# Kernel optimization log

Measured on AMD Instinct MI355X. Metric: run time of the kernel, lower is better.

## Reference

```python
import jax, jax.numpy as jnp
import numpy as np

POOLSCALE = 4  # HSA: avg-pool kernel/stride = (scale, scale*4)

def _avg_pool(x, kh, kw):
    # kernel == stride and dims divisible -> exact reshape-mean pooling
    B, C, H, W = x.shape
    return x.reshape(B, C, H // kh, kh, W // kw, kw).mean(axis=(3, 5))

def setup_inputs() -> dict:
    key = jax.random.key(0)
    k1, k2, k3 = jax.random.split(key, 3)
    shape = (4, 64, 192, 192)
    return {
        "K": jax.random.normal(k1, shape, dtype=jnp.float32),
        "Q": jax.random.normal(k2, shape, dtype=jnp.float32),
        "V": jax.random.normal(k3, shape, dtype=jnp.float32),
    }

def reference(K, Q, V):
    B, C, H, W = Q.shape
    kh, kw = POOLSCALE, POOLSCALE * 4
    Qp = Q.reshape(B, C, H * W).transpose(0, 2, 1)          # [B, HW, C]
    Kp = _avg_pool(K, kh, kw)                               # [B, C, h, w]
    Kp = Kp.reshape(B, C, -1)                               # [B, C, hw_p]
    Vp = _avg_pool(V, kh, kw).reshape(B, C, -1)             # [B, C, hw_p]
    scores = jnp.einsum('bnc,bcm->bnm', Qp, Kp)             # [B, HW, hw_p]
    attn = jax.nn.softmax(scores, axis=1)                   # softmax over query dim (dim=1), as in torch code
    out = jnp.einsum('bcm,bnm->bcn', Vp, attn)              # V_pie @ attn^T -> [B, C, HW]
    return out.reshape(B, C, H, W)
```

## Files before the change

### kernel.cpp

```cpp
#include <hip/hip_runtime.h>

#define BB 4
#define CC 64
#define HH 192
#define WW 192
#define HWN (HH*WW)
#define KH 4
#define KW 16
#define PW (WW/KW)
#define MP ((HH/KH)*(WW/KW))
#define NT 128
#define MT 64
#define MITER (MP/MT)
#define SCALE_W 65536.0f
#define INV_SCALE (1.0f/65536.0f)

typedef _Float16 half8 __attribute__((ext_vector_type(8)));
typedef _Float16 half4 __attribute__((ext_vector_type(4)));
typedef float floatx4 __attribute__((ext_vector_type(4)));


__global__ __launch_bounds__(256) void pool_kernel(
    const float* __restrict__ Kin, const float* __restrict__ Vin,
    _Float16* __restrict__ kptF, float* __restrict__ vp) {
  int t = blockIdx.x * 256 + threadIdx.x;
  const int total = BB * CC * MP;
  bool isV = t >= total;
  int idx = isV ? t - total : t;
  int m = idx % MP;
  int c = (idx / MP) % CC;
  int b = idx / (MP * CC);
  int mh = m / PW, mw = m % PW;
  const float* src = (isV ? Vin : Kin) + (((b * CC + c) * HH + mh * KH) * WW + mw * KW);
  float s = 0.f;
#pragma unroll
  for (int r = 0; r < KH; ++r) {
    const float4* row = (const float4*)(src + r * WW);
#pragma unroll
    for (int j = 0; j < KW / 4; ++j) {
      float4 v = row[j];
      s += v.x + v.y + v.z + v.w;
    }
  }
  s *= (1.0f / (KH * KW));
  if (isV) {
    vp[(b * CC + c) * MP + m] = s;
  } else {
    int mi = m >> 6, mloc = m & 63, l15 = mloc >> 2, mf = mloc & 3;
    int ks = c >> 5, lhi = (c >> 3) & 3, e = c & 7;
    int lane = lhi * 16 + l15;
    kptF[(((((b * MITER + mi) * 4 + mf) * 2 + ks)) * 64 + lane) * 8 + e] = (_Float16)s;
  }
}

__global__ __launch_bounds__(256) void colsum_kernel(
    const float* __restrict__ Q, const _Float16* __restrict__ kptF,
    float* __restrict__ colsum) {
  __shared__ float cs[MP];
  int b = blockIdx.y;
  int n0 = blockIdx.x * NT;
  int tid = threadIdx.x;
  int wv = tid >> 6;
  int lane = tid & 63;
  int l15 = lane & 15, lhi = lane >> 4;

  for (int i = tid; i < MP; i += 256) cs[i] = 0.f;
  __syncthreads();

  const float* Qb = Q + b * CC * HWN;
  int nrow = n0 + wv * 32 + l15;
  half8 afrag[2][2];
#pragma unroll
  for (int nf = 0; nf < 2; ++nf)
#pragma unroll
    for (int ks = 0; ks < 2; ++ks) {
      int cbase = ks * 32 + lhi * 8;
      int n = nrow + nf * 16;
#pragma unroll
      for (int e = 0; e < 8; ++e)
        afrag[nf][ks][e] = (_Float16)Qb[(cbase + e) * HWN + n];
    }

  const _Float16* kb = kptF + b * MITER * 8 * 512;
  floatx4 zero = {0.f, 0.f, 0.f, 0.f};

  half8 bb[2][4][2];
  floatx4 sacc[2][2][4];

#pragma unroll
  for (int mf = 0; mf < 4; ++mf)
#pragma unroll
    for (int ks = 0; ks < 2; ++ks)
      bb[0][mf][ks] = *(const half8*)(kb + ((0 * 4 + mf) * 2 + ks) * 512 + lane * 8);
#pragma unroll
  for (int mf = 0; mf < 4; ++mf)
#pragma unroll
    for (int ks = 0; ks < 2; ++ks)
      bb[1][mf][ks] = *(const half8*)(kb + ((1 * 4 + mf) * 2 + ks) * 512 + lane * 8);

#pragma unroll
  for (int nf = 0; nf < 2; ++nf)
#pragma unroll
    for (int mf = 0; mf < 4; ++mf) sacc[0][nf][mf] = zero;
  __builtin_amdgcn_s_setprio(1);
#pragma unroll
  for (int ks = 0; ks < 2; ++ks)
#pragma unroll
    for (int nf = 0; nf < 2; ++nf)
#pragma unroll
      for (int mf = 0; mf < 4; ++mf)
        sacc[0][nf][mf] = __builtin_amdgcn_mfma_f32_16x16x32_f16(
            afrag[nf][ks], bb[0][mf][ks], sacc[0][nf][mf], 0, 0, 0);
  __builtin_amdgcn_s_setprio(0);

#pragma unroll
  for (int mi = 1; mi <= 8; ++mi) {
    int cur = mi & 1, prv = (mi - 1) & 1;
    if (mi + 1 <= 8) {
#pragma unroll
      for (int mf = 0; mf < 4; ++mf)
#pragma unroll
        for (int ks = 0; ks < 2; ++ks)
          bb[(mi + 1) & 1][mf][ks] =
              *(const half8*)(kb + (((mi + 1) * 4 + mf) * 2 + ks) * 512 + lane * 8);
    }
#pragma unroll
    for (int nf = 0; nf < 2; ++nf)
#pragma unroll
      for (int mf = 0; mf < 4; ++mf) sacc[cur][nf][mf] = zero;
    __builtin_amdgcn_s_setprio(1);
#pragma unroll
    for (int ks = 0; ks < 2; ++ks)
#pragma unroll
      for (int nf = 0; nf < 2; ++nf)
#pragma unroll
        for (int mf = 0; mf < 4; ++mf)
          sacc[cur][nf][mf] = __builtin_amdgcn_mfma_f32_16x16x32_f16(
              afrag[nf][ks], bb[cur][mf][ks], sacc[cur][nf][mf], 0, 0, 0);
    __builtin_amdgcn_s_setprio(0);
#pragma unroll
    for (int mf = 0; mf < 4; ++mf) {
      float s = 0.f;
#pragma unroll
      for (int nf = 0; nf < 2; ++nf)
#pragma unroll
        for (int r = 0; r < 4; ++r)
          s += __expf(sacc[prv][nf][mf][r]);
      s += __shfl_xor(s, 16);
      s += __shfl_xor(s, 32);
      if (lane < 16) atomicAdd(&cs[(mi - 1) * MT + l15 * 4 + mf], s);
    }
  }
#pragma unroll
  for (int mf = 0; mf < 4; ++mf) {
    float s = 0.f;
#pragma unroll
    for (int nf = 0; nf < 2; ++nf)
#pragma unroll
      for (int r = 0; r < 4; ++r)
        s += __expf(sacc[0][nf][mf][r]);
    s += __shfl_xor(s, 16);
    s += __shfl_xor(s, 32);
    if (lane < 16) atomicAdd(&cs[8 * MT + l15 * 4 + mf], s);
  }
  __syncthreads();
  for (int i = tid; i < MP; i += 256) atomicAdd(&colsum[b * MP + i], cs[i]);
}

__global__ __launch_bounds__(256) void wprep_kernel(
    const float* __restrict__ vp, const float* __restrict__ colsum,
    _Float16* __restrict__ wqF) {
  int t = blockIdx.x * 256 + threadIdx.x;
  int m = t % MP;
  int c = (t / MP) % CC;
  int b = t / (CC * MP);
  float w = vp[t] / colsum[b * MP + m] * SCALE_W;
  int cf = c >> 4, l15 = c & 15;
  int mi = m >> 6, mloc = m & 63;
  int ks = mloc >> 5, lhi = (mloc >> 3) & 3, e = mloc & 7;
  int lane = lhi * 16 + l15;
  wqF[((((b * MITER + mi) * 4 + cf) * 2 + ks) * 64 + lane) * 8 + e] = (_Float16)w;
}

__global__ __launch_bounds__(256) void attn_main_kernel(
    const float* __restrict__ Q, const _Float16* __restrict__ kptF,
    const _Float16* __restrict__ wqF, float* __restrict__ out) {
  __shared__ char elds[4 * 8192];
  int b = blockIdx.y;
  int n0 = blockIdx.x * NT;
  int tid = threadIdx.x;
  int wv = tid >> 6;
  int lane = tid & 63;
  int l15 = lane & 15, lhi = lane >> 4;
  char* eb0 = elds + wv * 8192;
  char* eb1 = eb0 + 4096;

  const float* Qb = Q + b * CC * HWN;
  int nrow = n0 + wv * 32 + l15;
  half8 afrag[2][2];
#pragma unroll
  for (int nf = 0; nf < 2; ++nf)
#pragma unroll
    for (int ks = 0; ks < 2; ++ks) {
      int cbase = ks * 32 + lhi * 8;
      int n = nrow + nf * 16;
#pragma unroll
      for (int e = 0; e < 8; ++e)
        afrag[nf][ks][e] = (_Float16)Qb[(cbase + e) * HWN + n];
    }

  floatx4 zero = {0.f, 0.f, 0.f, 0.f};
  floatx4 oacc[4][2];
#pragma unroll
  for (int cf = 0; cf < 4; ++cf)
#pragma unroll
    for (int nf = 0; nf < 2; ++nf) oacc[cf][nf] = zero;

  const _Float16* kb = kptF + b * MITER * 8 * 512;
  const _Float16* wb = wqF + b * MITER * 8 * 512;

  half8 bb[2][4][2];
  half8 ww[2][4][2];
  floatx4 sacc[2][4];

#pragma unroll
  for (int mf = 0; mf < 4; ++mf)
#pragma unroll
    for (int ks = 0; ks < 2; ++ks)
      bb[0][mf][ks] = *(const half8*)(kb + ((0 * 4 + mf) * 2 + ks) * 512 + lane * 8);
#pragma unroll
  for (int cf = 0; cf < 4; ++cf)
#pragma unroll
    for (int ks = 0; ks < 2; ++ks)
      ww[0][cf][ks] = *(const half8*)(wb + ((0 * 4 + cf) * 2 + ks) * 512 + lane * 8);

#pragma unroll
  for (int mf = 0; mf < 4; ++mf)
#pragma unroll
    for (int ks = 0; ks < 2; ++ks)
      bb[1][mf][ks] = *(const half8*)(kb + ((1 * 4 + mf) * 2 + ks) * 512 + lane * 8);
#pragma unroll
  for (int nf = 0; nf < 2; ++nf)
#pragma unroll
    for (int mf = 0; mf < 4; ++mf) sacc[nf][mf] = zero;
  __builtin_amdgcn_s_setprio(1);
#pragma unroll
  for (int ks = 0; ks < 2; ++ks)
#pragma unroll
    for (int nf = 0; nf < 2; ++nf)
#pragma unroll
      for (int mf = 0; mf < 4; ++mf)
        sacc[nf][mf] = __builtin_amdgcn_mfma_f32_16x16x32_f16(
            afrag[nf][ks], bb[0][mf][ks], sacc[nf][mf], 0, 0, 0);
  __builtin_amdgcn_s_setprio(0);
#pragma unroll
  for (int nf = 0; nf < 2; ++nf)
#pragma unroll
    for (int r = 0; r < 4; ++r) {
      int nl = nf * 16 + lhi * 4 + r;
      half4 h;
#pragma unroll
      for (int mf = 0; mf < 4; ++mf) h[mf] = (_Float16)__expf(sacc[nf][mf][r]);
      int byte = nl * 128 + ((((l15 >> 1) ^ (nl & 7))) << 4) + ((l15 & 1) << 3);
      *(half4*)(eb0 + byte) = h;
    }

#pragma unroll
  for (int mi = 1; mi <= 8; ++mi) {
    int cur = mi & 1, prv = (mi - 1) & 1;
    char* ebR = prv ? eb1 : eb0;
    char* ebW = cur ? eb1 : eb0;

    half8 ef[2][2];
#pragma unroll
    for (int nf = 0; nf < 2; ++nf)
#pragma unroll
      for (int ks = 0; ks < 2; ++ks) {
        int nl = nf * 16 + l15;
        int slot = (ks * 4 + lhi) ^ (nl & 7);
        ef[nf][ks] = *(const half8*)(ebR + nl * 128 + (slot << 4));
      }

    if (mi + 1 <= 8) {
#pragma unroll
      for (int mf = 0; mf < 4; ++mf)
#pragma unroll
        for (int ks = 0; ks < 2; ++ks)
          bb[(mi + 1) & 1][mf][ks] =
              *(const half8*)(kb + (((mi + 1) * 4 + mf) * 2 + ks) * 512 + lane * 8);
    }

#pragma unroll
    for (int nf = 0; nf < 2; ++nf)
#pragma unroll
      for (int mf = 0; mf < 4; ++mf) sacc[nf][mf] = zero;
    __builtin_amdgcn_s_setprio(1);
#pragma unroll
    for (int ks = 0; ks < 2; ++ks)
#pragma unroll
      for (int nf = 0; nf < 2; ++nf)
#pragma unroll
        for (int mf = 0; mf < 4; ++mf)
          sacc[nf][mf] = __builtin_amdgcn_mfma_f32_16x16x32_f16(
              afrag[nf][ks], bb[cur][mf][ks], sacc[nf][mf], 0, 0, 0);

#pragma unroll
    for (int ks = 0; ks < 2; ++ks)
#pragma unroll
      for (int cf = 0; cf < 4; ++cf)
#pragma unroll
        for (int nf = 0; nf < 2; ++nf)
          oacc[cf][nf] = __builtin_amdgcn_mfma_f32_16x16x32_f16(
              ww[prv][cf][ks], ef[nf][ks], oacc[cf][nf], 0, 0, 0);
    __builtin_amdgcn_s_setprio(0);

#pragma unroll
    for (int cf = 0; cf < 4; ++cf)
#pragma unroll
      for (int ks = 0; ks < 2; ++ks)
        ww[cur][cf][ks] = *(const half8*)(wb + ((mi * 4 + cf) * 2 + ks) * 512 + lane * 8);

#pragma unroll
    for (int nf = 0; nf < 2; ++nf)
#pragma unroll
      for (int r = 0; r < 4; ++r) {
        int nl = nf * 16 + lhi * 4 + r;
        half4 h;
#pragma unroll
        for (int mf = 0; mf < 4; ++mf) h[mf] = (_Float16)__expf(sacc[nf][mf][r]);
        int byte = nl * 128 + ((((l15 >> 1) ^ (nl & 7))) << 4) + ((l15 & 1) << 3);
        *(half4*)(ebW + byte) = h;
      }
  }

  {
    half8 ef[2][2];
#pragma unroll
    for (int nf = 0; nf < 2; ++nf)
#pragma unroll
      for (int ks = 0; ks < 2; ++ks) {
        int nl = nf * 16 + l15;
        int slot = (ks * 4 + lhi) ^ (nl & 7);
        ef[nf][ks] = *(const half8*)(eb0 + nl * 128 + (slot << 4));
      }
    __builtin_amdgcn_s_setprio(1);
#pragma unroll
    for (int ks = 0; ks < 2; ++ks)
#pragma unroll
      for (int cf = 0; cf < 4; ++cf)
#pragma unroll
        for (int nf = 0; nf < 2; ++nf)
          oacc[cf][nf] = __builtin_amdgcn_mfma_f32_16x16x32_f16(
              ww[0][cf][ks], ef[nf][ks], oacc[cf][nf], 0, 0, 0);
    __builtin_amdgcn_s_setprio(0);
  }

  float* ob = out + b * CC * HWN;
#pragma unroll
  for (int cf = 0; cf < 4; ++cf)
#pragma unroll
    for (int nf = 0; nf < 2; ++nf)
#pragma unroll
      for (int r = 0; r < 4; ++r) {
        int c = cf * 16 + lhi * 4 + r;
        int n = n0 + wv * 32 + nf * 16 + l15;
        ob[c * HWN + n] = oacc[cf][nf][r] * INV_SCALE;
      }
}

extern "C" void kernel_launch(void* const* d_in, const int* in_sizes, int n_in,
                              void* d_out, int out_size, void* d_ws, size_t ws_size,
                              hipStream_t stream) {
  const float* K = (const float*)d_in[0];
  const float* Q = (const float*)d_in[1];
  const float* V = (const float*)d_in[2];
  float* out = (float*)d_out;
  char* ws = (char*)d_ws;
  _Float16* kptF  = (_Float16*)(ws);
  float*    vp    = (float*)(ws + 294912);
  _Float16* wqF   = (_Float16*)(ws + 294912 + 589824);
  float*    colsum = (float*)(ws + 294912 + 589824 + 294912);

  hipMemsetAsync(colsum, 0, BB * MP * sizeof(float), stream);
  pool_kernel<<<(2 * BB * CC * MP) / 256, 256, 0, stream>>>(K, V, kptF, vp);
  colsum_kernel<<<dim3(HWN / NT, BB), 256, 0, stream>>>(Q, kptF, colsum);
  wprep_kernel<<<(BB * CC * MP) / 256, 256, 0, stream>>>(vp, colsum, wqF);
  attn_main_kernel<<<dim3(HWN / NT, BB), 256, 0, stream>>>(Q, kptF, wqF, out);
}
```

Measured before the change: 101.9 us.

## Stage K and W tiles into LDS with async global_load_lds triple buffering

In both the colsum and main attention kernels, every wave used to load the per-batch K (and W) fragments from global memory into its own registers. Now the block loads them cooperatively into a 3-stage LDS ring using direct global-to-LDS loads, with vmcnt waits and block barriers between stages, so each tile is fetched once per block instead of once per wave. The colsum kernel also drops the cross-lane shuffle reduction and lets every lane atomically add into the shared column sums. The cost is more LDS traffic and LDS atomics, an extra barrier per iteration, and a possible race: a wave can start overwriting a stage slot before other waves have finished reading it.

New measurement: 133.1 us. +30.5%, slower.

```diff
diff --git a/kernel.cpp b/kernel.cpp
--- a/kernel.cpp
+++ b/kernel.cpp
@@ -1,4 +1,5 @@
 #include <hip/hip_runtime.h>
+#include <stdint.h>
 
 #define BB 4
 #define CC 64
@@ -19,6 +20,13 @@
 typedef _Float16 half4 __attribute__((ext_vector_type(4)));
 typedef float floatx4 __attribute__((ext_vector_type(4)));
 
+static __device__ __forceinline__ void gload16(const void* g, void* l) {
+  __builtin_amdgcn_global_load_lds((const __attribute__((address_space(1))) void*)g,
+                                   (__attribute__((address_space(3))) void*)l, 16, 0, 0);
+}
+#define WAITCNT_VM(N) asm volatile("s_waitcnt vmcnt(" #N ")" ::: "memory")
+#define WAITCNT_LGKM0 asm volatile("s_waitcnt lgkmcnt(0)" ::: "memory")
+
 
 __global__ __launch_bounds__(256) void pool_kernel(
     const float* __restrict__ Kin, const float* __restrict__ Vin,
@@ -57,6 +65,7 @@
     const float* __restrict__ Q, const _Float16* __restrict__ kptF,
     float* __restrict__ colsum) {
   __shared__ float cs[MP];
+  __shared__ char stg[3 * 8192];
   int b = blockIdx.y;
   int n0 = blockIdx.x * NT;
   int tid = threadIdx.x;
@@ -65,7 +74,6 @@
   int l15 = lane & 15, lhi = lane >> 4;
 
   for (int i = tid; i < MP; i += 256) cs[i] = 0.f;
-  __syncthreads();
 
   const float* Qb = Q + b * CC * HWN;
   int nrow = n0 + wv * 32 + l15;
@@ -82,61 +90,50 @@
     }
 
   const _Float16* kb = kptF + b * MITER * 8 * 512;
+  {
+    int q0 = wv * 2;
+#pragma unroll
+    for (int j = 0; j < 2; ++j)
+      gload16(kb + 0 * 4096 + (q0 + j) * 512 + lane * 8, stg + 0 * 8192 + (q0 + j) * 1024);
+#pragma unroll
+    for (int j = 0; j < 2; ++j)
+      gload16(kb + 1 * 4096 + (q0 + j) * 512 + lane * 8, stg + 1 * 8192 + (q0 + j) * 1024);
+  }
+  WAITCNT_LGKM0;
+  WAITCNT_VM(2);
+  __builtin_amdgcn_sched_barrier(0);
+  __builtin_amdgcn_s_barrier();
+
   floatx4 zero = {0.f, 0.f, 0.f, 0.f};
-
-  half8 bb[2][4][2];
-  floatx4 sacc[2][2][4];
-
-#pragma unroll
-  for (int mf = 0; mf < 4; ++mf)
+#pragma unroll
+  for (int mi = 0; mi < MITER; ++mi) {
+    half8 bfr[4][2];
+#pragma unroll
+    for (int mf = 0; mf < 4; ++mf)
+#pragma unroll
+      for (int ks = 0; ks < 2; ++ks)
+        bfr[mf][ks] = *(const half8*)(stg + (mi % 3) * 8192 + (mf * 2 + ks) * 1024 + lane * 16);
+    if (mi + 2 < MITER) {
+      int q0 = wv * 2;
+#pragma unroll
+      for (int j = 0; j < 2; ++j)
+        gload16(kb + (mi + 2) * 4096 + (q0 + j) * 512 + lane * 8,
+                stg + ((mi + 2) % 3) * 8192 + (q0 + j) * 1024);
+    }
+    floatx4 sacc[2][4];
+#pragma unroll
+    for (int nf = 0; nf < 2; ++nf)
+#pragma unroll
+      for (int mf = 0; mf < 4; ++mf) sacc[nf][mf] = zero;
+    __builtin_amdgcn_s_setprio(1);
 #pragma unroll
     for (int ks = 0; ks < 2; ++ks)
-      bb[0][mf][ks] = *(const half8*)(kb + ((0 * 4 + mf) * 2 + ks) * 512 + lane * 8);
-#pragma unroll
-  for (int mf = 0; mf < 4; ++mf)
-#pragma unroll
-    for (int ks = 0; ks < 2; ++ks)
-      bb[1][mf][ks] = *(const half8*)(kb + ((1 * 4 + mf) * 2 + ks) * 512 + lane * 8);
-
-#pragma unroll
-  for (int nf = 0; nf < 2; ++nf)
-#pragma unroll
-    for (int mf = 0; mf < 4; ++mf) sacc[0][nf][mf] = zero;
-  __builtin_amdgcn_s_setprio(1);
-#pragma unroll
-  for (int ks = 0; ks < 2; ++ks)
-#pragma unroll
-    for (int nf = 0; nf < 2; ++nf)
-#pragma unroll
-      for (int mf = 0; mf < 4; ++mf)
-        sacc[0][nf][mf] = __builtin_amdgcn_mfma_f32_16x16x32_f16(
-            afrag[nf][ks], bb[0][mf][ks], sacc[0][nf][mf], 0, 0, 0);
-  __builtin_amdgcn_s_setprio(0);
-
-#pragma unroll
-  for (int mi = 1; mi <= 8; ++mi) {
-    int cur = mi & 1, prv = (mi - 1) & 1;
-    if (mi + 1 <= 8) {
-#pragma unroll
-      for (int mf = 0; mf < 4; ++mf)
-#pragma unroll
-        for (int ks = 0; ks < 2; ++ks)
-          bb[(mi + 1) & 1][mf][ks] =
-              *(const half8*)(kb + (((mi + 1) * 4 + mf) * 2 + ks) * 512 + lane * 8);
-    }
-#pragma unroll
-    for (int nf = 0; nf < 2; ++nf)
-#pragma unroll
-      for (int mf = 0; mf < 4; ++mf) sacc[cur][nf][mf] = zero;
-    __builtin_amdgcn_s_setprio(1);
-#pragma unroll
-    for (int ks = 0; ks < 2; ++ks)
 #pragma unroll
       for (int nf = 0; nf < 2; ++nf)
 #pragma unroll
         for (int mf = 0; mf < 4; ++mf)
-          sacc[cur][nf][mf] = __builtin_amdgcn_mfma_f32_16x16x32_f16(
-              afrag[nf][ks], bb[cur][mf][ks], sacc[cur][nf][mf], 0, 0, 0);
+          sacc[nf][mf] = __builtin_amdgcn_mfma_f32_16x16x32_f16(
+              afrag[nf][ks], bfr[mf][ks], sacc[nf][mf], 0, 0, 0);
     __builtin_amdgcn_s_setprio(0);
 #pragma unroll
     for (int mf = 0; mf < 4; ++mf) {
@@ -145,23 +142,14 @@
       for (int nf = 0; nf < 2; ++nf)
 #pragma unroll
         for (int r = 0; r < 4; ++r)
-          s += __expf(sacc[prv][nf][mf][r]);
-      s += __shfl_xor(s, 16);
-      s += __shfl_xor(s, 32);
-      if (lane < 16) atomicAdd(&cs[(mi - 1) * MT + l15 * 4 + mf], s);
-    }
-  }
-#pragma unroll
-  for (int mf = 0; mf < 4; ++mf) {
-    float s = 0.f;
-#pragma unroll
-    for (int nf = 0; nf < 2; ++nf)
-#pragma unroll
-      for (int r = 0; r < 4; ++r)
-        s += __expf(sacc[0][nf][mf][r]);
-    s += __shfl_xor(s, 16);
-    s += __shfl_xor(s, 32);
-    if (lane < 16) atomicAdd(&cs[8 * MT + l15 * 4 + mf], s);
+          s += __expf(sacc[nf][mf][r]);
+      atomicAdd(&cs[mi * MT + l15 * 4 + mf], s);
+    }
+    if (mi < MITER - 1) {
+      if (mi + 2 < MITER) { WAITCNT_VM(2); } else { WAITCNT_VM(0); }
+      __builtin_amdgcn_sched_barrier(0);
+      __builtin_amdgcn_s_barrier();
+    }
   }
   __syncthreads();
   for (int i = tid; i < MP; i += 256) atomicAdd(&colsum[b * MP + i], cs[i]);
@@ -185,14 +173,15 @@
 __global__ __launch_bounds__(256) void attn_main_kernel(
     const float* __restrict__ Q, const _Float16* __restrict__ kptF,
     const _Float16* __restrict__ wqF, float* __restrict__ out) {
-  __shared__ char elds[4 * 8192];
+  __shared__ char lds[3 * 16384 + 4 * 8192];
+  char* stg = lds;
   int b = blockIdx.y;
   int n0 = blockIdx.x * NT;
   int tid = threadIdx.x;
   int wv = tid >> 6;
   int lane = tid & 63;
   int l15 = lane & 15, lhi = lane >> 4;
-  char* eb0 = elds + wv * 8192;
+  char* eb0 = lds + 49152 + wv * 8192;
   char* eb1 = eb0 + 4096;
 
   const float* Qb = Q + b * CC * HWN;
@@ -219,77 +208,62 @@
   const _Float16* kb = kptF + b * MITER * 8 * 512;
   const _Float16* wb = wqF + b * MITER * 8 * 512;
 
-  half8 bb[2][4][2];
-  half8 ww[2][4][2];
-  floatx4 sacc[2][4];
-
-#pragma unroll
-  for (int mf = 0; mf < 4; ++mf)
-#pragma unroll
-    for (int ks = 0; ks < 2; ++ks)
-      bb[0][mf][ks] = *(const half8*)(kb + ((0 * 4 + mf) * 2 + ks) * 512 + lane * 8);
-#pragma unroll
-  for (int cf = 0; cf < 4; ++cf)
-#pragma unroll
-    for (int ks = 0; ks < 2; ++ks)
-      ww[0][cf][ks] = *(const half8*)(wb + ((0 * 4 + cf) * 2 + ks) * 512 + lane * 8);
-
-#pragma unroll
-  for (int mf = 0; mf < 4; ++mf)
-#pragma unroll
-    for (int ks = 0; ks < 2; ++ks)
-      bb[1][mf][ks] = *(const half8*)(kb + ((1 * 4 + mf) * 2 + ks) * 512 + lane * 8);
-#pragma unroll
-  for (int nf = 0; nf < 2; ++nf)
-#pragma unroll
-    for (int mf = 0; mf < 4; ++mf) sacc[nf][mf] = zero;
-  __builtin_amdgcn_s_setprio(1);
-#pragma unroll
-  for (int ks = 0; ks < 2; ++ks)
-#pragma unroll
-    for (int nf = 0; nf < 2; ++nf)
-#pragma unroll
-      for (int mf = 0; mf < 4; ++mf)
-        sacc[nf][mf] = __builtin_amdgcn_mfma_f32_16x16x32_f16(
-            afrag[nf][ks], bb[0][mf][ks], sacc[nf][mf], 0, 0, 0);
-  __builtin_amdgcn_s_setprio(0);
-#pragma unroll
-  for (int nf = 0; nf < 2; ++nf)
-#pragma unroll
-    for (int r = 0; r < 4; ++r) {
-      int nl = nf * 16 + lhi * 4 + r;
-      half4 h;
-#pragma unroll
-      for (int mf = 0; mf < 4; ++mf) h[mf] = (_Float16)__expf(sacc[nf][mf][r]);
-      int byte = nl * 128 + ((((l15 >> 1) ^ (nl & 7))) << 4) + ((l15 & 1) << 3);
-      *(half4*)(eb0 + byte) = h;
-    }
-
-#pragma unroll
-  for (int mi = 1; mi <= 8; ++mi) {
-    int cur = mi & 1, prv = (mi - 1) & 1;
-    char* ebR = prv ? eb1 : eb0;
-    char* ebW = cur ? eb1 : eb0;
-
+#define STAGE_T(t, s)                                                          \
+  {                                                                            \
+    int q0_ = wv * 4;                                                          \
+    _Pragma("unroll") for (int j_ = 0; j_ < 4; ++j_) {                         \
+      int q_ = q0_ + j_;                                                       \
+      const _Float16* srcp_ = (q_ < 8 ? kb + (t)*4096 + q_ * 512               \
+                                      : wb + (t)*4096 + (q_ - 8) * 512) +      \
+                              lane * 8;                                        \
+      gload16(srcp_, stg + (s)*16384 + q_ * 1024);                             \
+    }                                                                          \
+  }
+
+  STAGE_T(0, 0);
+  STAGE_T(1, 1);
+  WAITCNT_VM(4);
+  __builtin_amdgcn_sched_barrier(0);
+  __builtin_amdgcn_s_barrier();
+
+#pragma unroll
+  for (int mi = 0; mi < MITER; ++mi) {
+    const int sc = mi % 3;
+    const int sp = (mi + 2) % 3;
+    char* ebR = ((mi - 1) & 1) ? eb1 : eb0;
+    char* ebW = (mi & 1) ? eb1 : eb0;
+
+    half8 bfr[4][2];
+#pragma unroll
+    for (int mf = 0; mf < 4; ++mf)
+#pragma unroll
+      for (int ks = 0; ks < 2; ++ks)
+        bfr[mf][ks] = *(const half8*)(stg + sc * 16384 + (mf * 2 + ks) * 1024 + lane * 16);
+    half8 wfr[4][2];
     half8 ef[2][2];
-#pragma unroll
-    for (int nf = 0; nf < 2; ++nf)
-#pragma unroll
-      for (int ks = 0; ks < 2; ++ks) {
-        int nl = nf * 16 + l15;
-        int slot = (ks * 4 + lhi) ^ (nl & 7);
-        ef[nf][ks] = *(const half8*)(ebR + nl * 128 + (slot << 4));
-      }
-
-    if (mi + 1 <= 8) {
-#pragma unroll
-      for (int mf = 0; mf < 4; ++mf)
+    if (mi >= 1) {
+#pragma unroll
+      for (int cf = 0; cf < 4; ++cf)
 #pragma unroll
         for (int ks = 0; ks < 2; ++ks)
-          bb[(mi + 1) & 1][mf][ks] =
-              *(const half8*)(kb + (((mi + 1) * 4 + mf) * 2 + ks) * 512 + lane * 8);
-    }
-
+          wfr[cf][ks] = *(const half8*)(stg + sp * 16384 + 8192 + (cf * 2 + ks) * 1024 + lane * 16);
+#pragma unroll
+      for (int nf = 0; nf < 2; ++nf)
+#pragma unroll
+        for (int ks = 0; ks < 2; ++ks) {
+          int nl = nf * 16 + l15;
+          int slot = (ks * 4 + lhi) ^ (nl & 7);
+          ef[nf][ks] = *(const half8*)(ebR + nl * 128 + (slot << 4));
+        }
+    }
+
+    if (mi >= 1 && mi + 2 < MITER) {
+      WAITCNT_LGKM0;
+      __builtin_amdgcn_sched_barrier(0);
+    }
+    if (mi + 2 < MITER) STAGE_T(mi + 2, sp);
+
+    floatx4 sacc[2][4];
 #pragma unroll
     for (int nf = 0; nf < 2; ++nf)
 #pragma unroll
@@ -302,23 +276,18 @@
 #pragma unroll
         for (int mf = 0; mf < 4; ++mf)
           sacc[nf][mf] = __builtin_amdgcn_mfma_f32_16x16x32_f16(
-              afrag[nf][ks], bb[cur][mf][ks], sacc[nf][mf], 0, 0, 0);
-
-#pragma unroll
-    for (int ks = 0; ks < 2; ++ks)
-#pragma unroll
-      for (int cf = 0; cf < 4; ++cf)
-#pragma unroll
-        for (int nf = 0; nf < 2; ++nf)
-          oacc[cf][nf] = __builtin_amdgcn_mfma_f32_16x16x32_f16(
-              ww[prv][cf][ks], ef[nf][ks], oacc[cf][nf], 0, 0, 0);
+              afrag[nf][ks], bfr[mf][ks], sacc[nf][mf], 0, 0, 0);
+    if (mi >= 1) {
+#pragma unroll
+      for (int ks = 0; ks < 2; ++ks)
+#pragma unroll
+        for (int cf = 0; cf < 4; ++cf)
+#pragma unroll
+          for (int nf = 0; nf < 2; ++nf)
+            oacc[cf][nf] = __builtin_amdgcn_mfma_f32_16x16x32_f16(
+                wfr[cf][ks], ef[nf][ks], oacc[cf][nf], 0, 0, 0);
+    }
     __builtin_amdgcn_s_setprio(0);
-
-#pragma unroll
-    for (int cf = 0; cf < 4; ++cf)
-#pragma unroll
-      for (int ks = 0; ks < 2; ++ks)
-        ww[cur][cf][ks] = *(const half8*)(wb + ((mi * 4 + cf) * 2 + ks) * 512 + lane * 8);
 
 #pragma unroll
     for (int nf = 0; nf < 2; ++nf)
@@ -331,9 +300,21 @@
         int byte = nl * 128 + ((((l15 >> 1) ^ (nl & 7))) << 4) + ((l15 & 1) << 3);
         *(half4*)(ebW + byte) = h;
       }
+
+    if (mi < MITER - 1) {
+      if (mi + 2 < MITER) { WAITCNT_VM(4); } else { WAITCNT_VM(0); }
+      __builtin_amdgcn_sched_barrier(0);
+      __builtin_amdgcn_s_barrier();
+    }
   }
 
   {
+    half8 wfr[4][2];
+#pragma unroll
+    for (int cf = 0; cf < 4; ++cf)
+#pragma unroll
+      for (int ks = 0; ks < 2; ++ks)
+        wfr[cf][ks] = *(const half8*)(stg + 2 * 16384 + 8192 + (cf * 2 + ks) * 1024 + lane * 16);
     half8 ef[2][2];
 #pragma unroll
     for (int nf = 0; nf < 2; ++nf)
@@ -351,7 +332,7 @@
 #pragma unroll
         for (int nf = 0; nf < 2; ++nf)
           oacc[cf][nf] = __builtin_amdgcn_mfma_f32_16x16x32_f16(
-              ww[0][cf][ks], ef[nf][ks], oacc[cf][nf], 0, 0, 0);
+              wfr[cf][ks], ef[nf][ks], oacc[cf][nf], 0, 0, 0);
     __builtin_amdgcn_s_setprio(0);
   }
 
```
